# Kernel optimization log

Hardware: AMD Instinct MI355X
Metric: run time of the kernel (lower is better)

Reference implementation:

```python
import jax, jax.numpy as jnp
import numpy as np

N = 2708
IN_C = 1433
OUT_C = 64


def setup_inputs() -> dict:
    key = jax.random.key(0)
    k1, k2, k3, k4, k5, k6, k7 = jax.random.split(key, 7)
    X = jax.random.normal(k1, (N, IN_C), dtype=jnp.float32)
    A = jax.random.randint(k2, (N, N), 0, 2, dtype=jnp.int32)  # dense binary adjacency mask
    # Graph Fourier basis: orthonormal-ish random matrix (QR of gaussian)
    U = jnp.linalg.qr(jax.random.normal(k3, (N, N), dtype=jnp.float32))[0]
    s = 1.0 / np.sqrt(IN_C)
    W_K = jax.random.normal(k4, (OUT_C, IN_C), dtype=jnp.float32) * s
    W_Q = jax.random.normal(k5, (OUT_C, IN_C), dtype=jnp.float32) * s
    W_V = jax.random.normal(k6, (OUT_C, IN_C), dtype=jnp.float32) * s
    lmbd = jax.random.uniform(k7, (N, 1), dtype=jnp.float32)
    return {"X": X, "A": A, "U": U, "W_K": W_K, "W_Q": W_Q, "W_V": W_V, "lmbd": lmbd}


def reference(X, A, U, W_K, W_Q, W_V, lmbd):
    # Linear projections (torch nn.Linear: x @ W.T)
    K = X @ W_K.T  # [N, d]
    Q = X @ W_Q.T  # [N, d]
    V = X @ W_V.T  # [N, d]
    d_k = K.shape[-1]
    E = (Q @ K.T) / d_k  # [N, N]
    # spectral filtering: igft(lmbd * gft(E)) = U @ (lmbd * (U^T @ E))
    E = jnp.abs(U @ (lmbd * (U.T @ E)))
    # masked softmax over neighbors; dropout p=0 in eval mode (no-op)
    E_masked = jnp.where(A == 0, -jnp.inf, E)
    alpha = jax.nn.softmax(E_masked, axis=-1)
    H = alpha @ V  # [N, d]
    return H
```

## Files before the change

kernel.cpp:

```cpp
#include <hip/hip_runtime.h>

#define NV 2708
#define INC 1433
#define XCOLS 1472
#define UDIM 2752
#define PSTR 2720
#define BSTR 2752
#define SLAB ((size_t)(2752*64))
#define MWPR 88
#define NSP 8
#define NSU 22

typedef __attribute__((ext_vector_type(8))) short bf16x8;
typedef __attribute__((ext_vector_type(4))) float f32x4;
typedef __attribute__((ext_vector_type(4))) unsigned short u16x4;

__device__ __forceinline__ unsigned short f2bf(float f){
  union { float f; unsigned int i; } v; v.f = f;
  return (unsigned short)((v.i + 0x7fffu + ((v.i >> 16) & 1u)) >> 16);
}

__global__ __launch_bounds__(256) void convert_all(
    const float* __restrict__ X, const float* __restrict__ WK,
    const float* __restrict__ WQ, const float* __restrict__ WV,
    const float* __restrict__ U, const int* __restrict__ A,
    unsigned short* __restrict__ Xbf, unsigned short* __restrict__ Wbf,
    unsigned short* __restrict__ Ubf, unsigned int* __restrict__ Abits)
{
  const int bx = blockIdx.x;
  const int tid = threadIdx.x;
  if (bx < 2752){
    const int row = bx;
    unsigned short* dst = Ubf + (size_t)row*UDIM;
    if (row < NV){
      const float* src = U + (size_t)row*NV;
      for (int c4 = tid; c4 < 688; c4 += 256){
        float4 v = make_float4(0.f,0.f,0.f,0.f);
        if (c4 < 677) v = *(const float4*)(src + c4*4);
        u16x4 h = { f2bf(v.x), f2bf(v.y), f2bf(v.z), f2bf(v.w) };
        *(u16x4*)(dst + c4*4) = h;
      }
    } else {
      u16x4 zz = {0,0,0,0};
      for (int c4 = tid; c4 < 688; c4 += 256) *(u16x4*)(dst + c4*4) = zz;
    }
  } else if (bx < 5504){
    const int row = bx - 2752;
    unsigned short* dst = Xbf + (size_t)row*XCOLS;
    if (row < NV){
      const float* src = X + (size_t)row*INC;
      for (int c = tid; c < XCOLS; c += 256)
        dst[c] = (c < INC) ? f2bf(src[c]) : (unsigned short)0;
    } else {
      for (int c = tid; c < XCOLS; c += 256) dst[c] = 0;
    }
  } else if (bx < 5696){
    const int row = bx - 5504;
    const float* s = (row < 64) ? WK : (row < 128) ? WQ : WV;
    const float* src = s + (size_t)(row & 63)*INC;
    unsigned short* dst = Wbf + (size_t)row*XCOLS;
    for (int c = tid; c < XCOLS; c += 256)
      dst[c] = (c < INC) ? f2bf(src[c]) : (unsigned short)0;
  } else {
    const int i = bx - 5696;
    const int lane = tid & 63, wave = tid >> 6;
    const int* arow = A + (size_t)i*NV;
    unsigned int* drow = Abits + (size_t)i*MWPR;
    if (tid < 2) drow[86 + tid] = 0u;
    for (int g = wave; g < 43; g += 4){
      int j = g*64 + lane;
      int a = (j < NV) ? arow[j] : 0;
      unsigned long long m = __ballot(a != 0);
      if (lane == 0){
        drow[2*g]     = (unsigned int)m;
        drow[2*g + 1] = (unsigned int)(m >> 32);
      }
    }
  }
}

__global__ __launch_bounds__(256) void proj(
    const unsigned short* __restrict__ Xbf, const unsigned short* __restrict__ Wbf,
    float* __restrict__ part)
{
  __shared__ __align__(16) unsigned short At[64*72];
  __shared__ __align__(16) unsigned short Bt[64*72];
  const int tid = threadIdx.x;
  const int lane = tid & 63, wave = tid >> 6, quad = lane >> 4, lr = lane & 15;
  const int m0 = blockIdx.x * 64;
  const int s  = blockIdx.y, z = blockIdx.z;
  const int kbeg = s * 192, kend = min(kbeg + 192, XCOLS);
  const int wm = (wave & 1) * 32, wn = (wave >> 1) * 32;
  const unsigned short* Wz = Wbf + (size_t)z*64*XCOLS;
  const int srow = wave*8 + (lane >> 3), seg = lane & 7;
  f32x4 acc[2][2] = {};

  for (int k0 = kbeg; k0 < kend; k0 += 64){
    #pragma unroll
    for (int e = 0; e < 2; e++){
      int row = e*32 + srow;
      bf16x8 xa = *(const bf16x8*)(Xbf + (size_t)(m0+row)*XCOLS + k0 + seg*8);
      bf16x8 wb = *(const bf16x8*)(Wz  + (size_t)row*XCOLS      + k0 + seg*8);
      *(bf16x8*)&At[row*72 + seg*8] = xa;
      *(bf16x8*)&Bt[row*72 + seg*8] = wb;
    }
    __syncthreads();
    #pragma unroll
    for (int ks = 0; ks < 2; ks++){
      bf16x8 af[2], bv[2];
      #pragma unroll
      for (int t = 0; t < 2; t++){
        af[t] = *(const bf16x8*)&At[(wm + t*16 + lr)*72 + ks*32 + quad*8];
        bv[t] = *(const bf16x8*)&Bt[(wn + t*16 + lr)*72 + ks*32 + quad*8];
      }
      #pragma unroll
      for (int tm = 0; tm < 2; tm++)
        #pragma unroll
        for (int tn = 0; tn < 2; tn++)
          acc[tm][tn] = __builtin_amdgcn_mfma_f32_16x16x32_bf16(af[tm], bv[tn], acc[tm][tn], 0, 0, 0);
    }
    __syncthreads();
  }
  float* dst = part + (size_t)(z*NSP + s) * SLAB;
  #pragma unroll
  for (int tm = 0; tm < 2; tm++)
    #pragma unroll
    for (int tn = 0; tn < 2; tn++)
      #pragma unroll
      for (int e = 0; e < 4; e++)
        dst[(size_t)(m0 + wm + tm*16 + quad*4 + e)*64 + wn + tn*16 + lr] = acc[tm][tn][e];
}

__global__ __launch_bounds__(256) void reduce_proj(
    const float* __restrict__ part, unsigned short* __restrict__ K16f,
    unsigned short* __restrict__ QT16, unsigned short* __restrict__ VTf)
{
  int idx = blockIdx.x*256 + threadIdx.x;
  int z = blockIdx.y;
  int m = idx >> 6, c = idx & 63;
  const float* base = part + (size_t)z*NSP*SLAB + idx;
  float v = 0.f;
  #pragma unroll
  for (int s = 0; s < NSP; s++) v += base[s*SLAB];
  unsigned short h = (m < NV) ? f2bf(v) : (unsigned short)0;
  if (z == 0){
    if (m < 2720) K16f[((m>>4)*2 + (c>>5))*512 + (m&15)*32 + (c&31)] = h;
  } else if (z == 1){
    QT16[(size_t)c*BSTR + m] = h;
  } else {
    if (m < 2720) VTf[(m>>5)*2048 + c*32 + (m&31)] = h;
  }
}

__global__ __launch_bounds__(256) void gemmG(
    const unsigned short* __restrict__ Ubf, const unsigned short* __restrict__ QT,
    float* __restrict__ part)
{
  __shared__ __align__(16) unsigned short At[64*72];
  __shared__ __align__(16) unsigned short Bt[64*72];
  const int tid = threadIdx.x;
  const int lane = tid & 63, wave = tid >> 6, quad = lane >> 4, lr = lane & 15;
  const int m0 = blockIdx.x * 64;
  const int s  = blockIdx.y;
  const int kbeg = s * 128, kend = min(kbeg + 128, UDIM);
  const int wm = (wave & 1) * 32, wn = (wave >> 1) * 32;
  const int bc = tid >> 2, bseg = tid & 3;
  const int ml = (lane & 15)*4, koff = wave*16 + (lane >> 4);
  f32x4 acc[2][2] = {};

  for (int k0 = kbeg; k0 < kend; k0 += 64){
    #pragma unroll
    for (int e = 0; e < 4; e++){
      int kl = koff + e*4;
      u16x4 v = *(const u16x4*)(Ubf + (size_t)(k0+kl)*UDIM + m0 + ml);
      At[(ml+0)*72 + kl] = v[0];
      At[(ml+1)*72 + kl] = v[1];
      At[(ml+2)*72 + kl] = v[2];
      At[(ml+3)*72 + kl] = v[3];
    }
    {
      const unsigned short* q = QT + (size_t)bc*BSTR + k0 + bseg*16;
      *(bf16x8*)&Bt[bc*72 + bseg*16]     = *(const bf16x8*)(q);
      *(bf16x8*)&Bt[bc*72 + bseg*16 + 8] = *(const bf16x8*)(q + 8);
    }
    __syncthreads();
    #pragma unroll
    for (int ks = 0; ks < 2; ks++){
      bf16x8 af[2], bv[2];
      #pragma unroll
      for (int t = 0; t < 2; t++){
        af[t] = *(const bf16x8*)&At[(wm + t*16 + lr)*72 + ks*32 + quad*8];
        bv[t] = *(const bf16x8*)&Bt[(wn + t*16 + lr)*72 + ks*32 + quad*8];
      }
      #pragma unroll
      for (int tm = 0; tm < 2; tm++)
        #pragma unroll
        for (int tn = 0; tn < 2; tn++)
          acc[tm][tn] = __builtin_amdgcn_mfma_f32_16x16x32_bf16(af[tm], bv[tn], acc[tm][tn], 0, 0, 0);
    }
    __syncthreads();
  }
  float* dst = part + (size_t)s * SLAB;
  #pragma unroll
  for (int tm = 0; tm < 2; tm++)
    #pragma unroll
    for (int tn = 0; tn < 2; tn++)
      #pragma unroll
      for (int e = 0; e < 4; e++)
        dst[(size_t)(m0 + wm + tm*16 + quad*4 + e)*64 + wn + tn*16 + lr] = acc[tm][tn][e];
}

__global__ __launch_bounds__(256) void reduce_g(
    const float* __restrict__ part, const float* __restrict__ lm,
    unsigned short* __restrict__ G2T)
{
  int idx = blockIdx.x*256 + threadIdx.x;
  int m = idx >> 6, c = idx & 63;
  const float* base = part + idx;
  float v = 0.f;
  #pragma unroll
  for (int s = 0; s < NSU; s++) v += base[s*SLAB];
  unsigned short h = 0;
  if (m < NV) h = f2bf(v * lm[m] * (1.0f/64.0f));
  G2T[(size_t)c*BSTR + m] = h;
}

__global__ __launch_bounds__(256) void gemmF(
    const unsigned short* __restrict__ Ubf, const unsigned short* __restrict__ G2T,
    float* __restrict__ part)
{
  __shared__ __align__(16) unsigned short At[64*72];
  __shared__ __align__(16) unsigned short Bt[64*72];
  const int tid = threadIdx.x;
  const int lane = tid & 63, wave = tid >> 6, quad = lane >> 4, lr = lane & 15;
  const int m0 = blockIdx.x * 64;
  const int s  = blockIdx.y;
  const int kbeg = s * 128, kend = min(kbeg + 128, UDIM);
  const int wm = (wave & 1) * 32, wn = (wave >> 1) * 32;
  const int bc = tid >> 2, bseg = tid & 3;
  const int srow = wave*8 + (lane >> 3), seg = lane & 7;
  f32x4 acc[2][2] = {};

  for (int k0 = kbeg; k0 < kend; k0 += 64){
    #pragma unroll
    for (int e = 0; e < 2; e++){
      int row = e*32 + srow;
      bf16x8 ua = *(const bf16x8*)(Ubf + (size_t)(m0+row)*UDIM + k0 + seg*8);
      *(bf16x8*)&At[row*72 + seg*8] = ua;
    }
    {
      const unsigned short* g = G2T + (size_t)bc*BSTR + k0 + bseg*16;
      *(bf16x8*)&Bt[bc*72 + bseg*16]     = *(const bf16x8*)(g);
      *(bf16x8*)&Bt[bc*72 + bseg*16 + 8] = *(const bf16x8*)(g + 8);
    }
    __syncthreads();
    #pragma unroll
    for (int ks = 0; ks < 2; ks++){
      bf16x8 af[2], bv[2];
      #pragma unroll
      for (int t = 0; t < 2; t++){
        af[t] = *(const bf16x8*)&At[(wm + t*16 + lr)*72 + ks*32 + quad*8];
        bv[t] = *(const bf16x8*)&Bt[(wn + t*16 + lr)*72 + ks*32 + quad*8];
      }
      #pragma unroll
      for (int tm = 0; tm < 2; tm++)
        #pragma unroll
        for (int tn = 0; tn < 2; tn++)
          acc[tm][tn] = __builtin_amdgcn_mfma_f32_16x16x32_bf16(af[tm], bv[tn], acc[tm][tn], 0, 0, 0);
    }
    __syncthreads();
  }
  float* dst = part + (size_t)s * SLAB;
  #pragma unroll
  for (int tm = 0; tm < 2; tm++)
    #pragma unroll
    for (int tn = 0; tn < 2; tn++)
      #pragma unroll
      for (int e = 0; e < 4; e++)
        dst[(size_t)(m0 + wm + tm*16 + quad*4 + e)*64 + wn + tn*16 + lr] = acc[tm][tn][e];
}

__global__ __launch_bounds__(256) void fused_attn(
    const float* __restrict__ partF, const unsigned short* __restrict__ K16f,
    const unsigned int* __restrict__ Abits, const unsigned short* __restrict__ VTf,
    float* __restrict__ Hout)
{
  __shared__ __align__(16) unsigned short pbuf[8*PSTR];
  __shared__ __align__(16) unsigned short fbuf[8*64];
  __shared__ unsigned int mrow[8*MWPR];
  __shared__ float swave[4][8];
  __shared__ float rinv[8];
  const int tid  = threadIdx.x;
  const int lane = tid & 63, wave = tid >> 6;
  const int quad = lane >> 4, lr = lane & 15;
  const int i0 = blockIdx.x * 8;

  #pragma unroll
  for (int h = 0; h < 2; h++){
    int idx = h*256 + tid;
    const float* base = partF + (size_t)(i0 + (idx >> 6))*64 + (idx & 63);
    float v = 0.f;
    #pragma unroll
    for (int s = 0; s < NSU; s++) v += base[s*SLAB];
    fbuf[idx] = f2bf(v);
  }
  for (int idx = tid; idx < 8*MWPR; idx += 256){
    int r = idx / MWPR;
    unsigned int v = 0;
    if (i0 + r < NV) v = Abits[(size_t)(i0 + r)*MWPR + (idx - r*MWPR)];
    mrow[idx] = v;
  }
  __syncthreads();

  const bf16x8 af0 = *(const bf16x8*)&fbuf[(lr & 7)*64 + quad*8];
  const bf16x8 af1 = *(const bf16x8*)&fbuf[(lr & 7)*64 + 32 + quad*8];
  float psum[4] = {0.f, 0.f, 0.f, 0.f};
  {
    int t = wave;
    const unsigned short* kb = K16f + t*1024 + lr*32 + quad*8;
    bf16x8 b0 = *(const bf16x8*)(kb);
    bf16x8 b1 = *(const bf16x8*)(kb + 512);
    while (t < 170){
      int tn = t + 4;
      bf16x8 n0 = b0, n1 = b1;
      if (tn < 170){
        const unsigned short* nb = K16f + tn*1024 + lr*32 + quad*8;
        n0 = *(const bf16x8*)(nb);
        n1 = *(const bf16x8*)(nb + 512);
      }
      f32x4 sv = {};
      sv = __builtin_amdgcn_mfma_f32_16x16x32_bf16(af0, b0, sv, 0, 0, 0);
      sv = __builtin_amdgcn_mfma_f32_16x16x32_bf16(af1, b1, sv, 0, 0, 0);
      if (quad < 2){
        int col = t*16 + lr;
        int wsh = col >> 5, bit = col & 31;
        #pragma unroll
        for (int e = 0; e < 4; e++){
          int r = quad*4 + e;
          float p = 0.f;
          if ((mrow[r*MWPR + wsh] >> bit) & 1u) p = __expf(fabsf(sv[e]));
          psum[e] += p;
          pbuf[r*PSTR + col] = f2bf(p);
        }
      }
      b0 = n0; b1 = n1; t = tn;
    }
  }
  #pragma unroll
  for (int e = 0; e < 4; e++){
    float v = psum[e];
    #pragma unroll
    for (int o = 1; o <= 8; o <<= 1) v += __shfl_xor(v, o, 64);
    if (lr == 0 && quad < 2) swave[wave][quad*4 + e] = v;
  }
  __syncthreads();
  if (tid < 8){
    float sum = swave[0][tid] + swave[1][tid] + swave[2][tid] + swave[3][tid];
    rinv[tid] = (sum > 0.f) ? (1.f/sum) : 0.f;
  }
  __syncthreads();

  const int c0 = wave * 16;
  const int mr = lr & 7;
  f32x4 acc = {};
  {
    bf16x8 bv = *(const bf16x8*)&VTf[(c0 + lr)*32 + quad*8];
    for (int kt = 0; kt < 85; kt++){
      bf16x8 bn = bv;
      if (kt + 1 < 85) bn = *(const bf16x8*)&VTf[(kt+1)*2048 + (c0 + lr)*32 + quad*8];
      bf16x8 af = *(const bf16x8*)&pbuf[mr*PSTR + kt*32 + quad*8];
      acc = __builtin_amdgcn_mfma_f32_16x16x32_bf16(af, bv, acc, 0, 0, 0);
      bv = bn;
    }
  }
  if (quad < 2){
    #pragma unroll
    for (int e = 0; e < 4; e++){
      int r = quad*4 + e;
      int i = i0 + r;
      if (i < NV) Hout[(size_t)i*64 + c0 + lr] = acc[e] * rinv[r];
    }
  }
}

extern "C" void kernel_launch(void* const* d_in, const int* in_sizes, int n_in,
                              void* d_out, int out_size, void* d_ws, size_t ws_size,
                              hipStream_t stream){
  (void)in_sizes; (void)n_in; (void)out_size; (void)ws_size;
  const float* X  = (const float*)d_in[0];
  const int*   A  = (const int*)d_in[1];
  const float* U  = (const float*)d_in[2];
  const float* WK = (const float*)d_in[3];
  const float* WQ = (const float*)d_in[4];
  const float* WV = (const float*)d_in[5];
  const float* lm = (const float*)d_in[6];

  char* ws = (char*)d_ws;
  size_t off = 0;
  auto alloc = [&](size_t bytes){ size_t o = off; off = (off + bytes + 255) & ~(size_t)255; return o; };
  float*          part = (float*)(ws + alloc(24*SLAB*4));
  unsigned short* Ubf  = (unsigned short*)(ws + alloc((size_t)UDIM*UDIM*2));
  unsigned short* Xbf  = (unsigned short*)(ws + alloc((size_t)UDIM*XCOLS*2));
  unsigned short* Wbf  = (unsigned short*)(ws + alloc((size_t)192*XCOLS*2));
  unsigned short* K16f = (unsigned short*)(ws + alloc((size_t)170*1024*2));
  unsigned short* QT16 = (unsigned short*)(ws + alloc((size_t)64*BSTR*2));
  unsigned short* G2T  = (unsigned short*)(ws + alloc((size_t)64*BSTR*2));
  unsigned short* VTf  = (unsigned short*)(ws + alloc((size_t)85*2048*2));
  unsigned int*   Abits= (unsigned int*)(ws + alloc((size_t)NV*MWPR*4));

  convert_all<<<dim3(8404), 256, 0, stream>>>(X, WK, WQ, WV, U, A, Xbf, Wbf, Ubf, Abits);
  proj<<<dim3(43, NSP, 3), 256, 0, stream>>>(Xbf, Wbf, part);
  reduce_proj<<<dim3(688, 3), 256, 0, stream>>>(part, K16f, QT16, VTf);
  gemmG<<<dim3(43, NSU), 256, 0, stream>>>(Ubf, QT16, part);
  reduce_g<<<dim3(688), 256, 0, stream>>>(part, lm, G2T);
  gemmF<<<dim3(43, NSU), 256, 0, stream>>>(Ubf, G2T, part);
  fused_attn<<<dim3((NV + 7)/8), 256, 0, stream>>>(part, K16f, Abits, VTf, (float*)d_out);
}
```

Measured before the change: 196.4 us.

## Drop split-K for projections, halve split-K in U GEMMs, load fragments directly

Replaces the split-K projection GEMM and its reduction kernel with one kernel that computes the full K loop per block and writes the bf16 K/Q/V layouts directly, removing a launch and the fp32 partial round-trip. The U-side GEMMs move from 22 to 11 K splits, and operands that were staged through LDS are now read straight from global memory into MFMA fragments, which drops shared-memory traffic and barriers. The attention kernel's two chained MFMAs are split into independent accumulators to shorten the dependency chain. In exchange there are fewer blocks in flight for the projection and U GEMMs, and direct global fragment loads are less coalesced and give no reuse across waves.

Result: slower. 206.8 us (+5.3%).

```diff
diff --git a/kernel.cpp b/kernel.cpp
--- a/kernel.cpp
+++ b/kernel.cpp
@@ -8,8 +8,7 @@
 #define BSTR 2752
 #define SLAB ((size_t)(2752*64))
 #define MWPR 88
-#define NSP 8
-#define NSU 22
+#define NSU 11
 
 typedef __attribute__((ext_vector_type(8))) short bf16x8;
 typedef __attribute__((ext_vector_type(4))) float f32x4;
@@ -79,76 +78,46 @@
   }
 }
 
-__global__ __launch_bounds__(256) void proj(
+__global__ __launch_bounds__(256) void proj_direct(
     const unsigned short* __restrict__ Xbf, const unsigned short* __restrict__ Wbf,
-    float* __restrict__ part)
-{
-  __shared__ __align__(16) unsigned short At[64*72];
-  __shared__ __align__(16) unsigned short Bt[64*72];
+    unsigned short* __restrict__ K16f, unsigned short* __restrict__ QT16,
+    unsigned short* __restrict__ VTf)
+{
   const int tid = threadIdx.x;
   const int lane = tid & 63, wave = tid >> 6, quad = lane >> 4, lr = lane & 15;
-  const int m0 = blockIdx.x * 64;
-  const int s  = blockIdx.y, z = blockIdx.z;
-  const int kbeg = s * 192, kend = min(kbeg + 192, XCOLS);
-  const int wm = (wave & 1) * 32, wn = (wave >> 1) * 32;
-  const unsigned short* Wz = Wbf + (size_t)z*64*XCOLS;
-  const int srow = wave*8 + (lane >> 3), seg = lane & 7;
-  f32x4 acc[2][2] = {};
-
-  for (int k0 = kbeg; k0 < kend; k0 += 64){
-    #pragma unroll
-    for (int e = 0; e < 2; e++){
-      int row = e*32 + srow;
-      bf16x8 xa = *(const bf16x8*)(Xbf + (size_t)(m0+row)*XCOLS + k0 + seg*8);
-      bf16x8 wb = *(const bf16x8*)(Wz  + (size_t)row*XCOLS      + k0 + seg*8);
-      *(bf16x8*)&At[row*72 + seg*8] = xa;
-      *(bf16x8*)&Bt[row*72 + seg*8] = wb;
-    }
-    __syncthreads();
+  const int m0 = blockIdx.x * 32;
+  const int z  = blockIdx.y;
+  const int wm = (wave & 1) * 16, wn = (wave >> 1) * 32;
+  const unsigned short* xrow  = Xbf + (size_t)(m0 + wm + lr) * XCOLS;
+  const unsigned short* wrow0 = Wbf + (size_t)(z*64 + wn + lr) * XCOLS;
+  const unsigned short* wrow1 = Wbf + (size_t)(z*64 + wn + 16 + lr) * XCOLS;
+  f32x4 acc[2] = {};
+  for (int k0 = 0; k0 < XCOLS; k0 += 64){
     #pragma unroll
     for (int ks = 0; ks < 2; ks++){
-      bf16x8 af[2], bv[2];
-      #pragma unroll
-      for (int t = 0; t < 2; t++){
-        af[t] = *(const bf16x8*)&At[(wm + t*16 + lr)*72 + ks*32 + quad*8];
-        bv[t] = *(const bf16x8*)&Bt[(wn + t*16 + lr)*72 + ks*32 + quad*8];
-      }
-      #pragma unroll
-      for (int tm = 0; tm < 2; tm++)
-        #pragma unroll
-        for (int tn = 0; tn < 2; tn++)
-          acc[tm][tn] = __builtin_amdgcn_mfma_f32_16x16x32_bf16(af[tm], bv[tn], acc[tm][tn], 0, 0, 0);
-    }
-    __syncthreads();
-  }
-  float* dst = part + (size_t)(z*NSP + s) * SLAB;
-  #pragma unroll
-  for (int tm = 0; tm < 2; tm++)
-    #pragma unroll
-    for (int tn = 0; tn < 2; tn++)
-      #pragma unroll
-      for (int e = 0; e < 4; e++)
-        dst[(size_t)(m0 + wm + tm*16 + quad*4 + e)*64 + wn + tn*16 + lr] = acc[tm][tn][e];
-}
-
-__global__ __launch_bounds__(256) void reduce_proj(
-    const float* __restrict__ part, unsigned short* __restrict__ K16f,
-    unsigned short* __restrict__ QT16, unsigned short* __restrict__ VTf)
-{
-  int idx = blockIdx.x*256 + threadIdx.x;
-  int z = blockIdx.y;
-  int m = idx >> 6, c = idx & 63;
-  const float* base = part + (size_t)z*NSP*SLAB + idx;
-  float v = 0.f;
-  #pragma unroll
-  for (int s = 0; s < NSP; s++) v += base[s*SLAB];
-  unsigned short h = (m < NV) ? f2bf(v) : (unsigned short)0;
-  if (z == 0){
-    if (m < 2720) K16f[((m>>4)*2 + (c>>5))*512 + (m&15)*32 + (c&31)] = h;
-  } else if (z == 1){
-    QT16[(size_t)c*BSTR + m] = h;
-  } else {
-    if (m < 2720) VTf[(m>>5)*2048 + c*32 + (m&31)] = h;
+      int ko = k0 + ks*32 + quad*8;
+      bf16x8 af = *(const bf16x8*)(xrow  + ko);
+      bf16x8 b0 = *(const bf16x8*)(wrow0 + ko);
+      bf16x8 b1 = *(const bf16x8*)(wrow1 + ko);
+      acc[0] = __builtin_amdgcn_mfma_f32_16x16x32_bf16(af, b0, acc[0], 0, 0, 0);
+      acc[1] = __builtin_amdgcn_mfma_f32_16x16x32_bf16(af, b1, acc[1], 0, 0, 0);
+    }
+  }
+  #pragma unroll
+  for (int tn = 0; tn < 2; tn++){
+    #pragma unroll
+    for (int e = 0; e < 4; e++){
+      int m = m0 + wm + quad*4 + e;
+      int c = wn + tn*16 + lr;
+      unsigned short h = f2bf(acc[tn][e]);
+      if (z == 0){
+        if (m < 2720) K16f[((m>>4)*2 + (c>>5))*512 + (m&15)*32 + (c&31)] = h;
+      } else if (z == 1){
+        QT16[(size_t)c*BSTR + m] = h;
+      } else {
+        if (m < 2720) VTf[(m>>5)*2048 + c*32 + (m&31)] = h;
+      }
+    }
   }
 }
 
@@ -157,14 +126,12 @@
     float* __restrict__ part)
 {
   __shared__ __align__(16) unsigned short At[64*72];
-  __shared__ __align__(16) unsigned short Bt[64*72];
   const int tid = threadIdx.x;
   const int lane = tid & 63, wave = tid >> 6, quad = lane >> 4, lr = lane & 15;
   const int m0 = blockIdx.x * 64;
   const int s  = blockIdx.y;
-  const int kbeg = s * 128, kend = min(kbeg + 128, UDIM);
+  const int kbeg = s * 256, kend = min(kbeg + 256, UDIM);
   const int wm = (wave & 1) * 32, wn = (wave >> 1) * 32;
-  const int bc = tid >> 2, bseg = tid & 3;
   const int ml = (lane & 15)*4, koff = wave*16 + (lane >> 4);
   f32x4 acc[2][2] = {};
 
@@ -178,25 +145,24 @@
       At[(ml+2)*72 + kl] = v[2];
       At[(ml+3)*72 + kl] = v[3];
     }
-    {
-      const unsigned short* q = QT + (size_t)bc*BSTR + k0 + bseg*16;
-      *(bf16x8*)&Bt[bc*72 + bseg*16]     = *(const bf16x8*)(q);
-      *(bf16x8*)&Bt[bc*72 + bseg*16 + 8] = *(const bf16x8*)(q + 8);
-    }
+    bf16x8 bv[2][2];
+    #pragma unroll
+    for (int ks = 0; ks < 2; ks++)
+      #pragma unroll
+      for (int t = 0; t < 2; t++)
+        bv[ks][t] = *(const bf16x8*)(QT + (size_t)(wn + t*16 + lr)*BSTR + k0 + ks*32 + quad*8);
     __syncthreads();
     #pragma unroll
     for (int ks = 0; ks < 2; ks++){
-      bf16x8 af[2], bv[2];
-      #pragma unroll
-      for (int t = 0; t < 2; t++){
+      bf16x8 af[2];
+      #pragma unroll
+      for (int t = 0; t < 2; t++)
         af[t] = *(const bf16x8*)&At[(wm + t*16 + lr)*72 + ks*32 + quad*8];
-        bv[t] = *(const bf16x8*)&Bt[(wn + t*16 + lr)*72 + ks*32 + quad*8];
-      }
       #pragma unroll
       for (int tm = 0; tm < 2; tm++)
         #pragma unroll
         for (int tn = 0; tn < 2; tn++)
-          acc[tm][tn] = __builtin_amdgcn_mfma_f32_16x16x32_bf16(af[tm], bv[tn], acc[tm][tn], 0, 0, 0);
+          acc[tm][tn] = __builtin_amdgcn_mfma_f32_16x16x32_bf16(af[tm], bv[ks][tn], acc[tm][tn], 0, 0, 0);
     }
     __syncthreads();
   }
@@ -229,46 +195,31 @@
     const unsigned short* __restrict__ Ubf, const unsigned short* __restrict__ G2T,
     float* __restrict__ part)
 {
-  __shared__ __align__(16) unsigned short At[64*72];
-  __shared__ __align__(16) unsigned short Bt[64*72];
   const int tid = threadIdx.x;
   const int lane = tid & 63, wave = tid >> 6, quad = lane >> 4, lr = lane & 15;
   const int m0 = blockIdx.x * 64;
   const int s  = blockIdx.y;
-  const int kbeg = s * 128, kend = min(kbeg + 128, UDIM);
+  const int kbeg = s * 256, kend = min(kbeg + 256, UDIM);
   const int wm = (wave & 1) * 32, wn = (wave >> 1) * 32;
-  const int bc = tid >> 2, bseg = tid & 3;
-  const int srow = wave*8 + (lane >> 3), seg = lane & 7;
+  const unsigned short* ua0 = Ubf + (size_t)(m0 + wm + lr) * UDIM;
+  const unsigned short* ua1 = Ubf + (size_t)(m0 + wm + 16 + lr) * UDIM;
+  const unsigned short* gb0 = G2T + (size_t)(wn + lr) * BSTR;
+  const unsigned short* gb1 = G2T + (size_t)(wn + 16 + lr) * BSTR;
   f32x4 acc[2][2] = {};
 
   for (int k0 = kbeg; k0 < kend; k0 += 64){
     #pragma unroll
-    for (int e = 0; e < 2; e++){
-      int row = e*32 + srow;
-      bf16x8 ua = *(const bf16x8*)(Ubf + (size_t)(m0+row)*UDIM + k0 + seg*8);
-      *(bf16x8*)&At[row*72 + seg*8] = ua;
-    }
-    {
-      const unsigned short* g = G2T + (size_t)bc*BSTR + k0 + bseg*16;
-      *(bf16x8*)&Bt[bc*72 + bseg*16]     = *(const bf16x8*)(g);
-      *(bf16x8*)&Bt[bc*72 + bseg*16 + 8] = *(const bf16x8*)(g + 8);
-    }
-    __syncthreads();
-    #pragma unroll
     for (int ks = 0; ks < 2; ks++){
-      bf16x8 af[2], bv[2];
-      #pragma unroll
-      for (int t = 0; t < 2; t++){
-        af[t] = *(const bf16x8*)&At[(wm + t*16 + lr)*72 + ks*32 + quad*8];
-        bv[t] = *(const bf16x8*)&Bt[(wn + t*16 + lr)*72 + ks*32 + quad*8];
-      }
-      #pragma unroll
-      for (int tm = 0; tm < 2; tm++)
-        #pragma unroll
-        for (int tn = 0; tn < 2; tn++)
-          acc[tm][tn] = __builtin_amdgcn_mfma_f32_16x16x32_bf16(af[tm], bv[tn], acc[tm][tn], 0, 0, 0);
-    }
-    __syncthreads();
+      int ko = k0 + ks*32 + quad*8;
+      bf16x8 a0 = *(const bf16x8*)(ua0 + ko);
+      bf16x8 a1 = *(const bf16x8*)(ua1 + ko);
+      bf16x8 b0 = *(const bf16x8*)(gb0 + ko);
+      bf16x8 b1 = *(const bf16x8*)(gb1 + ko);
+      acc[0][0] = __builtin_amdgcn_mfma_f32_16x16x32_bf16(a0, b0, acc[0][0], 0, 0, 0);
+      acc[0][1] = __builtin_amdgcn_mfma_f32_16x16x32_bf16(a0, b1, acc[0][1], 0, 0, 0);
+      acc[1][0] = __builtin_amdgcn_mfma_f32_16x16x32_bf16(a1, b0, acc[1][0], 0, 0, 0);
+      acc[1][1] = __builtin_amdgcn_mfma_f32_16x16x32_bf16(a1, b1, acc[1][1], 0, 0, 0);
+    }
   }
   float* dst = part + (size_t)s * SLAB;
   #pragma unroll
@@ -328,9 +279,10 @@
         n0 = *(const bf16x8*)(nb);
         n1 = *(const bf16x8*)(nb + 512);
       }
-      f32x4 sv = {};
-      sv = __builtin_amdgcn_mfma_f32_16x16x32_bf16(af0, b0, sv, 0, 0, 0);
-      sv = __builtin_amdgcn_mfma_f32_16x16x32_bf16(af1, b1, sv, 0, 0, 0);
+      f32x4 sv0 = {}, sv1 = {};
+      sv0 = __builtin_amdgcn_mfma_f32_16x16x32_bf16(af0, b0, sv0, 0, 0, 0);
+      sv1 = __builtin_amdgcn_mfma_f32_16x16x32_bf16(af1, b1, sv1, 0, 0, 0);
+      f32x4 sv = sv0 + sv1;
       if (quad < 2){
         int col = t*16 + lr;
         int wsh = col >> 5, bit = col & 31;
@@ -398,7 +350,7 @@
   char* ws = (char*)d_ws;
   size_t off = 0;
   auto alloc = [&](size_t bytes){ size_t o = off; off = (off + bytes + 255) & ~(size_t)255; return o; };
-  float*          part = (float*)(ws + alloc(24*SLAB*4));
+  float*          part = (float*)(ws + alloc((size_t)NSU*SLAB*4));
   unsigned short* Ubf  = (unsigned short*)(ws + alloc((size_t)UDIM*UDIM*2));
   unsigned short* Xbf  = (unsigned short*)(ws + alloc((size_t)UDIM*XCOLS*2));
   unsigned short* Wbf  = (unsigned short*)(ws + alloc((size_t)192*XCOLS*2));
@@ -409,8 +361,7 @@
   unsigned int*   Abits= (unsigned int*)(ws + alloc((size_t)NV*MWPR*4));
 
   convert_all<<<dim3(8404), 256, 0, stream>>>(X, WK, WQ, WV, U, A, Xbf, Wbf, Ubf, Abits);
-  proj<<<dim3(43, NSP, 3), 256, 0, stream>>>(Xbf, Wbf, part);
-  reduce_proj<<<dim3(688, 3), 256, 0, stream>>>(part, K16f, QT16, VTf);
+  proj_direct<<<dim3(86, 3), 256, 0, stream>>>(Xbf, Wbf, K16f, QT16, VTf);
   gemmG<<<dim3(43, NSU), 256, 0, stream>>>(Ubf, QT16, part);
   reduce_g<<<dim3(688), 256, 0, stream>>>(part, lm, G2T);
   gemmF<<<dim3(43, NSU), 256, 0, stream>>>(Ubf, G2T, part);
```
